# Kernel tuning notes

Hardware: AMD Instinct MI355X
Metric: run time of the kernel (lower is better)

The kernel has to match this reference:

```python
import jax, jax.numpy as jnp
import numpy as np

N_NODES = 100000
N_EDGES = 1600000
IN_DIM = 256
OUT_DIM = 128
SELF_LOOP_W = 2.0  # improved=True


def setup_inputs() -> dict:
    key = jax.random.key(0)
    ks = jax.random.split(key, 9)
    x = jax.random.normal(ks[0], (N_NODES, IN_DIM), dtype=jnp.float32)
    edge_index = jax.random.randint(ks[1], (2, N_EDGES), 0, N_NODES, dtype=jnp.int64)
    edge_weight = jax.random.uniform(ks[2], (N_EDGES,), dtype=jnp.float32)
    s1 = 1.0 / np.sqrt(IN_DIM)
    s2 = 1.0 / np.sqrt(OUT_DIM)
    W1 = jax.random.normal(ks[3], (IN_DIM, OUT_DIM), dtype=jnp.float32) * s1
    b1 = jnp.zeros((OUT_DIM,), dtype=jnp.float32)
    W_mu = jax.random.normal(ks[4], (OUT_DIM, OUT_DIM), dtype=jnp.float32) * s2
    b_mu = jnp.zeros((OUT_DIM,), dtype=jnp.float32)
    W_var = jax.random.normal(ks[5], (OUT_DIM, OUT_DIM), dtype=jnp.float32) * s2
    b_var = jnp.zeros((OUT_DIM,), dtype=jnp.float32)
    return {"x": x, "edge_index": edge_index, "edge_weight": edge_weight,
            "W1": W1, "b1": b1, "W_mu": W_mu, "b_mu": b_mu,
            "W_var": W_var, "b_var": b_var}


def _gcn_norm(edge_index, edge_weight, num_nodes):
    # add self loops with fill value 2.0 (improved=True), then symmetric norm
    loop = jnp.arange(num_nodes, dtype=edge_index.dtype)
    row = jnp.concatenate([edge_index[0], loop])
    col = jnp.concatenate([edge_index[1], loop])
    ew = jnp.concatenate([edge_weight,
                          jnp.full((num_nodes,), SELF_LOOP_W, dtype=edge_weight.dtype)])
    deg = jax.ops.segment_sum(ew, col, num_segments=num_nodes)
    dis = jnp.where(deg > 0, jax.lax.rsqrt(jnp.where(deg > 0, deg, 1.0)), 0.0)
    norm = dis[row] * ew * dis[col]
    return row, col, norm


def _gcn_conv(x, row, col, norm, W, b, num_nodes):
    xw = x @ W                      # [N, out]
    msg = xw[row] * norm[:, None]   # [E+N, out] per-edge messages
    out = jax.ops.segment_sum(msg, col, num_segments=num_nodes)
    return out + b


def reference(x, edge_index, edge_weight, W1, b1, W_mu, b_mu, W_var, b_var):
    n = x.shape[0]
    row, col, norm = _gcn_norm(edge_index, edge_weight, n)
    feat = jax.nn.relu(_gcn_conv(x, row, col, norm, W1, b1, n))
    mu = _gcn_conv(feat, row, col, norm, W_mu, b_mu, n)
    var = _gcn_conv(feat, row, col, norm, W_var, b_var, n)
    return (mu, var)
```

## Files before the change

### kernel.cpp

```cpp
#include <hip/hip_runtime.h>
#include <hip/hip_bf16.h>

#define CDIV(a,b) (((a)+(b)-1)/(b))

typedef __attribute__((ext_vector_type(8))) short short8;
typedef __attribute__((ext_vector_type(4))) float f32x4;

static __device__ inline short f2bf(float f) {
    union { __hip_bfloat16 h; short s; } u;
    u.h = __float2bfloat16(f);
    return u.s;
}
static __device__ inline ushort f2bfu(float f) { return (ushort)f2bf(f); }
static __device__ inline float bfu_lo(uint v) { return __uint_as_float(v << 16); }
static __device__ inline float bfu_hi(uint v) { return __uint_as_float(v & 0xffff0000u); }


__global__ __launch_bounds__(512) void k_init(const float* __restrict__ W1,
                                              short* __restrict__ W1t,
                                              const float* __restrict__ Wmu,
                                              const float* __restrict__ Wvar,
                                              short* __restrict__ Wcat) {
    int i = blockIdx.x * 512 + threadIdx.x;
    if (i < 128 * 256) {
        int k = i % 256, col = i / 256;
        W1t[i] = f2bf(W1[(size_t)k * 128 + col]);
    } else if (i < 2 * 128 * 256) {
        int j = i - 128 * 256;
        int k = j & 127, col = j >> 7;
        float v = (col < 128) ? Wmu[(size_t)k * 128 + col] : Wvar[(size_t)k * 128 + (col - 128)];
        Wcat[j] = f2bf(v);
    }
}


__global__ __launch_bounds__(512) void k_fat(const float* __restrict__ A,
                                             const short* __restrict__ Bt,
                                             ushort* __restrict__ C, int n, int nGB,
                                             const int* __restrict__ coli,
                                             int* __restrict__ bhist,
                                             int E, int chunkBH, int nbk, int NBH) {
    const int K = 256, KH = 128;
    __shared__ short Blds[128 * KH];
    int t = threadIdx.x;

    if (blockIdx.x >= nGB) {
        int* h = (int*)Blds;
        int b = blockIdx.x - nGB;
        for (int i = t; i < nbk; i += 512) h[i] = 0;
        __syncthreads();
        int e0 = b * chunkBH, e1 = min(E, e0 + chunkBH);
        for (int e = e0 + t; e < e1; e += 512)
            atomicAdd(&h[coli[e] >> 8], 1);
        __syncthreads();
        for (int i = t; i < nbk; i += 512)
            bhist[i * NBH + b] = h[i];
        return;
    }

    int wave = t >> 6, lane = t & 63;
    int lg = lane >> 4, lr = lane & 15;
    long row_base = (long)blockIdx.x * 256 + wave * 32;

    long ra0 = row_base + lr;      if (ra0 > n - 1) ra0 = n - 1;
    long ra1 = row_base + 16 + lr; if (ra1 > n - 1) ra1 = n - 1;

    f32x4 acc[2][8];
    #pragma unroll
    for (int i = 0; i < 2; ++i)
        #pragma unroll
        for (int j = 0; j < 8; ++j) acc[i][j] = (f32x4){0.f, 0.f, 0.f, 0.f};

    const float* pa0 = A + ra0 * K + lg * 8;
    const float* pa1 = A + ra1 * K + lg * 8;

    #pragma unroll
    for (int p = 0; p < 2; ++p) {
        if (p) __syncthreads();
        const int CHK = KH / 8;
        for (int c = t; c < 128 * CHK; c += 512) {
            int colw = c / CHK;
            int kb  = (c % CHK) * 16;
            int dst = colw * (KH * 2) + (kb ^ ((colw & 7) << 4));
            *(float4*)((char*)Blds + dst) =
                *(const float4*)((const char*)Bt + (size_t)colw * (K * 2) + p * (KH * 2) + kb);
        }
        __syncthreads();

        for (int k0 = 0; k0 < KH; k0 += 32) {
            int kg = p * KH + k0;
            float4 x0 = *(const float4*)(pa0 + kg);
            float4 x1 = *(const float4*)(pa0 + kg + 4);
            float4 y0 = *(const float4*)(pa1 + kg);
            float4 y1 = *(const float4*)(pa1 + kg + 4);
            short8 a0, a1;
            a0[0]=f2bf(x0.x); a0[1]=f2bf(x0.y); a0[2]=f2bf(x0.z); a0[3]=f2bf(x0.w);
            a0[4]=f2bf(x1.x); a0[5]=f2bf(x1.y); a0[6]=f2bf(x1.z); a0[7]=f2bf(x1.w);
            a1[0]=f2bf(y0.x); a1[1]=f2bf(y0.y); a1[2]=f2bf(y0.z); a1[3]=f2bf(y0.w);
            a1[4]=f2bf(y1.x); a1[5]=f2bf(y1.y); a1[6]=f2bf(y1.z); a1[7]=f2bf(y1.w);

            int kb = (k0 + lg * 8) * 2;
            #pragma unroll
            for (int cb = 0; cb < 8; ++cb) {
                int colm = cb * 16 + lr;
                short8 bfr = *(short8*)((char*)Blds + colm * (KH * 2) + (kb ^ ((colm & 7) << 4)));
                acc[0][cb] = __builtin_amdgcn_mfma_f32_16x16x32_bf16(a0, bfr, acc[0][cb], 0, 0, 0);
                acc[1][cb] = __builtin_amdgcn_mfma_f32_16x16x32_bf16(a1, bfr, acc[1][cb], 0, 0, 0);
            }
        }
    }

    #pragma unroll
    for (int rf = 0; rf < 2; ++rf) {
        #pragma unroll
        for (int cb = 0; cb < 8; ++cb) {
            int colm = cb * 16 + lr;
            #pragma unroll
            for (int r = 0; r < 4; ++r) {
                long row = row_base + rf * 16 + lg * 4 + r;
                if (row < n) C[row * 128 + colm] = f2bfu(acc[rf][cb][r]);
            }
        }
    }
}


__global__ __launch_bounds__(256) void kscanA(const int* __restrict__ in,
                                              int* __restrict__ out,
                                              int* __restrict__ part, int n) {
    int t = threadIdx.x;
    int base = blockIdx.x * 1024 + t * 4;
    int v0 = (base + 0 < n) ? in[base + 0] : 0;
    int v1 = (base + 1 < n) ? in[base + 1] : 0;
    int v2 = (base + 2 < n) ? in[base + 2] : 0;
    int v3 = (base + 3 < n) ? in[base + 3] : 0;
    int tsum = v0 + v1 + v2 + v3;
    int lane = t & 63, wv = t >> 6;
    int val = tsum;
    #pragma unroll
    for (int d = 1; d < 64; d <<= 1) {
        int u = __shfl_up(val, d, 64);
        if (lane >= d) val += u;
    }
    __shared__ int ws[4];
    if (lane == 63) ws[wv] = val;
    __syncthreads();
    int woff = 0;
    #pragma unroll
    for (int i = 0; i < 4; ++i) if (i < wv) woff += ws[i];
    int excl = woff + val - tsum;
    if (base + 0 < n) out[base + 0] = excl;  excl += v0;
    if (base + 1 < n) out[base + 1] = excl;  excl += v1;
    if (base + 2 < n) out[base + 2] = excl;  excl += v2;
    if (base + 3 < n) out[base + 3] = excl;
    if (t == 255) part[blockIdx.x] = woff + val;
}

__global__ __launch_bounds__(128) void kscanB(int* part, int nb) {
    int t = threadIdx.x;
    int v = (t < nb) ? part[t] : 0;
    int lane = t & 63, wv = t >> 6;
    int val = v;
    #pragma unroll
    for (int d = 1; d < 64; d <<= 1) {
        int u = __shfl_up(val, d, 64);
        if (lane >= d) val += u;
    }
    __shared__ int ws[2];
    if (lane == 63) ws[wv] = val;
    __syncthreads();
    int woff = (wv == 1) ? ws[0] : 0;
    if (t < nb) part[t] = woff + val - v;
}

__global__ __launch_bounds__(512) void k_bucket(const int* __restrict__ rowi,
                                                const int* __restrict__ coli,
                                                const float* __restrict__ ew,
                                                const int* __restrict__ excl,
                                                const int* __restrict__ part,
                                                int2* __restrict__ bxw,
                                                int E, int chunk, int nbk) {
    __shared__ int cur[512];
    int b = blockIdx.x, t = threadIdx.x, nblk = gridDim.x;
    for (int i = t; i < nbk; i += 512) cur[i] = 0;
    __syncthreads();
    int e0 = b * chunk, e1 = min(E, e0 + chunk);
    for (int e = e0 + t; e < e1; e += 512) {
        int c = coli[e];
        int bk = c >> 8;
        int idx = bk * nblk + b;
        int pos = excl[idx] + part[idx >> 10] + atomicAdd(&cur[bk], 1);
        bxw[pos] = make_int2(((c & 255) << 17) | rowi[e], __float_as_int(ew[e]));
    }
}

__global__ __launch_bounds__(512) void k_fine2(const int2* __restrict__ bxw,
                                               const int* __restrict__ excl,
                                               const int* __restrict__ part,
                                               int* __restrict__ row_ptr,
                                               float* __restrict__ dis,
                                               int E, int nblk, int n) {
    __shared__ int cnt[256], ews[256];
    __shared__ int ws2[4];
    int bk = blockIdx.x, t = threadIdx.x;
    if (t < 256) { cnt[t] = 0; ews[t] = 0; }
    __syncthreads();
    int i0 = bk * nblk;
    int s0 = excl[i0] + part[i0 >> 10];
    int s1 = E;
    if (bk + 1 < gridDim.x) {
        int i1 = (bk + 1) * nblk;
        s1 = excl[i1] + part[i1 >> 10];
    }
    for (int p = s0 + t; p < s1; p += 512) {
        int2 u = bxw[p];
        int cl = u.x >> 17;
        atomicAdd(&cnt[cl], 1);
        int q = (int)(__int_as_float(u.y) * 16777216.0f + 0.5f);
        atomicAdd(&ews[cl], q);
    }
    __syncthreads();
    int v = 0, val = 0;
    int lane = t & 63, wv = t >> 6;
    if (t < 256) {
        v = cnt[t];
        val = v;
        #pragma unroll
        for (int d = 1; d < 64; d <<= 1) {
            int u = __shfl_up(val, d, 64);
            if (lane >= d) val += u;
        }
        if (lane == 63) ws2[wv] = val;
    }
    __syncthreads();
    if (t < 256) {
        int woff = 0;
        #pragma unroll
        for (int i = 0; i < 4; ++i) if (i < wv) woff += ws2[i];
        int lexcl = woff + val - v;
        int c = bk * 256 + t;
        if (c < n) {
            row_ptr[c] = s0 + lexcl;
            dis[c] = rsqrtf(2.0f + (float)ews[t] * (1.0f / 16777216.0f));
        }
    }
    if (bk == 0 && t == 0) row_ptr[n] = E;
}

__global__ __launch_bounds__(512) void k_place(const int2* __restrict__ bxw,
                                               const int* __restrict__ excl,
                                               const int* __restrict__ part,
                                               const int* __restrict__ row_ptr,
                                               const float* __restrict__ dis,
                                               int2* __restrict__ csr,
                                               int E, int nblk, int n) {
    __shared__ int cur[256];
    int bk = blockIdx.x, t = threadIdx.x;
    if (t < 256) cur[t] = 0;
    __syncthreads();
    int i0 = bk * nblk;
    int s0 = excl[i0] + part[i0 >> 10];
    int s1 = E;
    if (bk + 1 < gridDim.x) {
        int i1 = (bk + 1) * nblk;
        s1 = excl[i1] + part[i1 >> 10];
    }
    int cbase = bk * 256;
    for (int p = s0 + t; p < s1; p += 512) {
        int2 u = bxw[p];
        int cl = u.x >> 17, r = u.x & 0x1FFFF;
        int pos = row_ptr[cbase + cl] + atomicAdd(&cur[cl], 1);
        csr[pos] = make_int2(r, __float_as_int(dis[r] * __int_as_float(u.y)));
    }
}


template<int OUTMODE>
__global__ __launch_bounds__(128) void k_agg(const uint2* __restrict__ src,
                                             const int* __restrict__ row_ptr,
                                             const int2* __restrict__ csr,
                                             const float* __restrict__ dis,
                                             const float* __restrict__ bias,
                                             uint2* __restrict__ dst, int n) {
    int wid = (blockIdx.x * 128 + threadIdx.x) >> 6;
    int lane = threadIdx.x & 63;
    int hb = lane >> 5, lc = lane & 31;
    if (wid >= n) return;
    int e0 = row_ptr[wid], e1 = row_ptr[wid + 1];

    float p00=0.f,p01=0.f,p02=0.f,p03=0.f;
    float p10=0.f,p11=0.f,p12=0.f,p13=0.f;
    float p20=0.f,p21=0.f,p22=0.f,p23=0.f;
    float p30=0.f,p31=0.f,p32=0.f,p33=0.f;

    int e = e0;
    for (; e + 7 < e1; e += 8) {
        int2 c0 = csr[e     + hb];
        int2 c1 = csr[e + 2 + hb];
        int2 c2 = csr[e + 4 + hb];
        int2 c3 = csr[e + 6 + hb];
        uint2 v0 = src[(size_t)c0.x * 32 + lc];
        uint2 v1 = src[(size_t)c1.x * 32 + lc];
        uint2 v2 = src[(size_t)c2.x * 32 + lc];
        uint2 v3 = src[(size_t)c3.x * 32 + lc];
        float w0 = __int_as_float(c0.y), w1 = __int_as_float(c1.y);
        float w2 = __int_as_float(c2.y), w3 = __int_as_float(c3.y);
        p00 += w0 * bfu_lo(v0.x); p01 += w0 * bfu_hi(v0.x);
        p02 += w0 * bfu_lo(v0.y); p03 += w0 * bfu_hi(v0.y);
        p10 += w1 * bfu_lo(v1.x); p11 += w1 * bfu_hi(v1.x);
        p12 += w1 * bfu_lo(v1.y); p13 += w1 * bfu_hi(v1.y);
        p20 += w2 * bfu_lo(v2.x); p21 += w2 * bfu_hi(v2.x);
        p22 += w2 * bfu_lo(v2.y); p23 += w2 * bfu_hi(v2.y);
        p30 += w3 * bfu_lo(v3.x); p31 += w3 * bfu_hi(v3.x);
        p32 += w3 * bfu_lo(v3.y); p33 += w3 * bfu_hi(v3.y);
    }
    for (; e + 1 < e1; e += 2) {
        int2 c = csr[e + hb];
        uint2 v = src[(size_t)c.x * 32 + lc];
        float w = __int_as_float(c.y);
        p00 += w * bfu_lo(v.x); p01 += w * bfu_hi(v.x);
        p02 += w * bfu_lo(v.y); p03 += w * bfu_hi(v.y);
    }
    if (e < e1 && hb == 0) {
        int2 c = csr[e];
        uint2 v = src[(size_t)c.x * 32 + lc];
        float w = __int_as_float(c.y);
        p10 += w * bfu_lo(v.x); p11 += w * bfu_hi(v.x);
        p12 += w * bfu_lo(v.y); p13 += w * bfu_hi(v.y);
    }

    float x0 = (p00 + p10) + (p20 + p30);
    float x1 = (p01 + p11) + (p21 + p31);
    float x2 = (p02 + p12) + (p22 + p32);
    float x3 = (p03 + p13) + (p23 + p33);
    x0 = x0 + __shfl_xor(x0, 32);
    x1 = x1 + __shfl_xor(x1, 32);
    x2 = x2 + __shfl_xor(x2, 32);
    x3 = x3 + __shfl_xor(x3, 32);

    float dc = dis[wid];
    uint2 sv = src[(size_t)wid * 32 + lc];
    float sw = 2.f * dc * dc;
    float o0 = dc * x0 + sw * bfu_lo(sv.x);
    float o1 = dc * x1 + sw * bfu_hi(sv.x);
    float o2 = dc * x2 + sw * bfu_lo(sv.y);
    float o3 = dc * x3 + sw * bfu_hi(sv.y);
    if constexpr (OUTMODE == 0) {
        float4 bv = *(const float4*)(bias + lc * 4);
        o0 += bv.x; o1 += bv.y; o2 += bv.z; o3 += bv.w;
        o0 = fmaxf(o0, 0.f); o1 = fmaxf(o1, 0.f);
        o2 = fmaxf(o2, 0.f); o3 = fmaxf(o3, 0.f);
    }
    if (hb == 0)
        dst[(size_t)wid * 32 + lc] =
            make_uint2((uint)f2bfu(o0) | ((uint)f2bfu(o1) << 16),
                       (uint)f2bfu(o2) | ((uint)f2bfu(o3) << 16));
}


__global__ __launch_bounds__(512) void k_gemm2(const short* __restrict__ A,
                                               const short* __restrict__ Bt,
                                               const float* __restrict__ bmu,
                                               const float* __restrict__ bvar,
                                               float* __restrict__ out,
                                               int n) {
    const int K = 128;
    __shared__ short Blds[256 * K];
    int t = threadIdx.x;

    const int CHK = K / 8;
    for (int c = t; c < 256 * CHK; c += 512) {
        int col = c / CHK;
        int kb  = (c % CHK) * 16;
        int dst = col * (K * 2) + (kb ^ ((col & 7) << 4));
        *(float4*)((char*)Blds + dst) =
            *(const float4*)((const char*)Bt + (size_t)col * (K * 2) + kb);
    }
    __syncthreads();

    int wave = t >> 6, lane = t & 63;
    int lg = lane >> 4, lr = lane & 15;
    int colbase = (wave & 1) * 128;
    long row_base = (long)blockIdx.x * 128 + (wave >> 1) * 32;

    long ra0 = row_base + lr;      if (ra0 > n - 1) ra0 = n - 1;
    long ra1 = row_base + 16 + lr; if (ra1 > n - 1) ra1 = n - 1;

    f32x4 acc[2][8];
    #pragma unroll
    for (int i = 0; i < 2; ++i)
        #pragma unroll
        for (int j = 0; j < 8; ++j) acc[i][j] = (f32x4){0.f, 0.f, 0.f, 0.f};

    const short* pa0 = A + ra0 * K + lg * 8;
    const short* pa1 = A + ra1 * K + lg * 8;

    #pragma unroll
    for (int k0 = 0; k0 < K; k0 += 32) {
        short8 a0 = *(const short8*)(pa0 + k0);
        short8 a1 = *(const short8*)(pa1 + k0);
        int kb = (k0 + lg * 8) * 2;
        #pragma unroll
        for (int cb = 0; cb < 8; ++cb) {
            int col = colbase + cb * 16 + lr;
            short8 b = *(short8*)((char*)Blds + col * (K * 2) + (kb ^ ((col & 7) << 4)));
            acc[0][cb] = __builtin_amdgcn_mfma_f32_16x16x32_bf16(a0, b, acc[0][cb], 0, 0, 0);
            acc[1][cb] = __builtin_amdgcn_mfma_f32_16x16x32_bf16(a1, b, acc[1][cb], 0, 0, 0);
        }
    }

    #pragma unroll
    for (int rf = 0; rf < 2; ++rf) {
        #pragma unroll
        for (int cb = 0; cb < 8; ++cb) {
            int colc = colbase + cb * 16 + lr;
            bool is_var = colc >= 128;
            int col = is_var ? colc - 128 : colc;
            float bv = is_var ? bvar[col] : bmu[col];
            size_t obase = is_var ? (size_t)n * 128 : 0;
            #pragma unroll
            for (int r = 0; r < 4; ++r) {
                long row = row_base + rf * 16 + lg * 4 + r;
                if (row < n)
                    __builtin_nontemporal_store(acc[rf][cb][r] + bv,
                                                &out[obase + (size_t)row * 128 + col]);
            }
        }
    }
}


extern "C" void kernel_launch(void* const* d_in, const int* in_sizes, int n_in,
                              void* d_out, int out_size, void* d_ws, size_t ws_size,
                              hipStream_t stream) {
    const float* x    = (const float*)d_in[0];
    const int*   ei   = (const int*)d_in[1];
    const float* ew   = (const float*)d_in[2];
    const float* W1   = (const float*)d_in[3];
    const float* b1   = (const float*)d_in[4];
    const float* Wmu  = (const float*)d_in[5];
    const float* bmu  = (const float*)d_in[6];
    const float* Wvar = (const float*)d_in[7];
    const float* bvar = (const float*)d_in[8];

    const int E = in_sizes[2];
    const int N = in_sizes[0] / 256;
    const int* rowi = ei;
    const int* coli = ei + E;

    char* base = (char*)d_ws;
    size_t off = 0;
    auto alloc = [&](size_t bytes) -> void* {
        void* p = base + off;
        off = (off + bytes + 511) & ~(size_t)511;
        return p;
    };
    const int NBH  = 256;
    const int nbk  = CDIV(N, 256);
    const int nh   = nbk * NBH;
    const int nGB  = CDIV(N, 256);
    const int chunkBH = CDIV(E, NBH);

    int*   bhist   = (int*)  alloc((size_t)nh * 4);
    int*   excl    = (int*)  alloc((size_t)nh * 4);
    int*   part    = (int*)  alloc(256 * 4);
    int2*  bxw     = (int2*) alloc((size_t)E * 8);
    int*   row_ptr = (int*)  alloc((size_t)(N + 1) * 4);
    float* dis     = (float*)alloc((size_t)N * 4);
    int2*  csr     = (int2*) alloc((size_t)E * 8);
    uint*  xw      = (uint*) alloc((size_t)N * 64 * 4);
    uint*  feat    = (uint*) alloc((size_t)N * 64 * 4);
    short* W1t     = (short*)alloc((size_t)256 * 128 * 2);
    short* Wcat    = (short*)alloc((size_t)256 * 128 * 2);
    uint*  g       = xw;

    k_init<<<CDIV(2 * 128 * 256, 512), 512, 0, stream>>>(W1, W1t, Wmu, Wvar, Wcat);

    k_fat<<<nGB + NBH, 512, 0, stream>>>(x, W1t, (ushort*)xw, N, nGB,
                                         coli, bhist, E, chunkBH, nbk, NBH);

    kscanA<<<CDIV(nh, 1024), 256, 0, stream>>>(bhist, excl, part, nh);
    kscanB<<<1, 128, 0, stream>>>(part, CDIV(nh, 1024));
    k_bucket<<<NBH, 512, 0, stream>>>(rowi, coli, ew, excl, part, bxw, E, chunkBH, nbk);
    k_fine2<<<nbk, 512, 0, stream>>>(bxw, excl, part, row_ptr, dis, E, NBH, N);
    k_place<<<nbk, 512, 0, stream>>>(bxw, excl, part, row_ptr, dis, csr, E, NBH, N);

    k_agg<0><<<CDIV(N * 64, 128), 128, 0, stream>>>((const uint2*)xw, row_ptr, csr, dis, b1, (uint2*)feat, N);
    k_agg<1><<<CDIV(N * 64, 128), 128, 0, stream>>>((const uint2*)feat, row_ptr, csr, dis, nullptr, (uint2*)g, N);
    k_gemm2<<<CDIV(N, 128), 512, 0, stream>>>((const short*)g, Wcat, bmu, bvar, (float*)d_out, N);
}
```

Measured before the change: 254.5 us.

## Drop separate part-scan kernel and halve GEMM rows per block

Removes the kscanB launch by having each consumer kernel (k_bucket, k_fine2, k_place) redundantly scan the block partial sums in shared memory. This saves one kernel launch and its serialization gap at the cost of a small duplicate scan in every block. The first GEMM in k_fat now gives each wave 16 rows instead of 32, so the grid has twice as many GEMM blocks. That raises parallelism but also doubles the LDS staging of the weight matrix relative to the useful work.

```diff
diff --git a/kernel.cpp b/kernel.cpp
--- a/kernel.cpp
+++ b/kernel.cpp
@@ -60,19 +60,15 @@
 
     int wave = t >> 6, lane = t & 63;
     int lg = lane >> 4, lr = lane & 15;
-    long row_base = (long)blockIdx.x * 256 + wave * 32;
-
-    long ra0 = row_base + lr;      if (ra0 > n - 1) ra0 = n - 1;
-    long ra1 = row_base + 16 + lr; if (ra1 > n - 1) ra1 = n - 1;
-
-    f32x4 acc[2][8];
-    #pragma unroll
-    for (int i = 0; i < 2; ++i)
-        #pragma unroll
-        for (int j = 0; j < 8; ++j) acc[i][j] = (f32x4){0.f, 0.f, 0.f, 0.f};
+    long row_base = (long)blockIdx.x * 128 + wave * 16;
+
+    long ra0 = row_base + lr; if (ra0 > n - 1) ra0 = n - 1;
+
+    f32x4 acc[8];
+    #pragma unroll
+    for (int j = 0; j < 8; ++j) acc[j] = (f32x4){0.f, 0.f, 0.f, 0.f};
 
     const float* pa0 = A + ra0 * K + lg * 8;
-    const float* pa1 = A + ra1 * K + lg * 8;
 
     #pragma unroll
     for (int p = 0; p < 2; ++p) {
@@ -91,35 +87,27 @@
             int kg = p * KH + k0;
             float4 x0 = *(const float4*)(pa0 + kg);
             float4 x1 = *(const float4*)(pa0 + kg + 4);
-            float4 y0 = *(const float4*)(pa1 + kg);
-            float4 y1 = *(const float4*)(pa1 + kg + 4);
-            short8 a0, a1;
+            short8 a0;
             a0[0]=f2bf(x0.x); a0[1]=f2bf(x0.y); a0[2]=f2bf(x0.z); a0[3]=f2bf(x0.w);
             a0[4]=f2bf(x1.x); a0[5]=f2bf(x1.y); a0[6]=f2bf(x1.z); a0[7]=f2bf(x1.w);
-            a1[0]=f2bf(y0.x); a1[1]=f2bf(y0.y); a1[2]=f2bf(y0.z); a1[3]=f2bf(y0.w);
-            a1[4]=f2bf(y1.x); a1[5]=f2bf(y1.y); a1[6]=f2bf(y1.z); a1[7]=f2bf(y1.w);
 
             int kb = (k0 + lg * 8) * 2;
             #pragma unroll
             for (int cb = 0; cb < 8; ++cb) {
                 int colm = cb * 16 + lr;
                 short8 bfr = *(short8*)((char*)Blds + colm * (KH * 2) + (kb ^ ((colm & 7) << 4)));
-                acc[0][cb] = __builtin_amdgcn_mfma_f32_16x16x32_bf16(a0, bfr, acc[0][cb], 0, 0, 0);
-                acc[1][cb] = __builtin_amdgcn_mfma_f32_16x16x32_bf16(a1, bfr, acc[1][cb], 0, 0, 0);
+                acc[cb] = __builtin_amdgcn_mfma_f32_16x16x32_bf16(a0, bfr, acc[cb], 0, 0, 0);
             }
         }
     }
 
     #pragma unroll
-    for (int rf = 0; rf < 2; ++rf) {
-        #pragma unroll
-        for (int cb = 0; cb < 8; ++cb) {
-            int colm = cb * 16 + lr;
-            #pragma unroll
-            for (int r = 0; r < 4; ++r) {
-                long row = row_base + rf * 16 + lg * 4 + r;
-                if (row < n) C[row * 128 + colm] = f2bfu(acc[rf][cb][r]);
-            }
+    for (int cb = 0; cb < 8; ++cb) {
+        int colm = cb * 16 + lr;
+        #pragma unroll
+        for (int r = 0; r < 4; ++r) {
+            long row = row_base + lg * 4 + r;
+            if (row < n) C[row * 128 + colm] = f2bfu(acc[cb][r]);
         }
     }
 }
@@ -156,61 +144,66 @@
     if (t == 255) part[blockIdx.x] = woff + val;
 }
 
-__global__ __launch_bounds__(128) void kscanB(int* part, int nb) {
+static __device__ inline void scan_parts(const int* __restrict__ part, int nparts,
+                                         int* pscan , int* wtot ) {
     int t = threadIdx.x;
-    int v = (t < nb) ? part[t] : 0;
-    int lane = t & 63, wv = t >> 6;
-    int val = v;
-    #pragma unroll
-    for (int d = 1; d < 64; d <<= 1) {
-        int u = __shfl_up(val, d, 64);
-        if (lane >= d) val += u;
-    }
-    __shared__ int ws[2];
-    if (lane == 63) ws[wv] = val;
-    __syncthreads();
-    int woff = (wv == 1) ? ws[0] : 0;
-    if (t < nb) part[t] = woff + val - v;
+    int lane = t & 63;
+    if (t < 128) {
+        int v = (t < nparts) ? part[t] : 0;
+        int val = v;
+        #pragma unroll
+        for (int d = 1; d < 64; d <<= 1) {
+            int u = __shfl_up(val, d, 64);
+            if (lane >= d) val += u;
+        }
+        if (lane == 63) wtot[t >> 6] = val;
+        pscan[t] = val - v;
+    }
+    __syncthreads();
+    if (t >= 64 && t < 128) pscan[t] += wtot[0];
+    __syncthreads();
 }
 
 __global__ __launch_bounds__(512) void k_bucket(const int* __restrict__ rowi,
                                                 const int* __restrict__ coli,
                                                 const float* __restrict__ ew,
                                                 const int* __restrict__ excl,
-                                                const int* __restrict__ part,
+                                                const int* __restrict__ part, int nparts,
                                                 int2* __restrict__ bxw,
                                                 int E, int chunk, int nbk) {
     __shared__ int cur[512];
+    __shared__ int pscan[128], wtot[2];
     int b = blockIdx.x, t = threadIdx.x, nblk = gridDim.x;
     for (int i = t; i < nbk; i += 512) cur[i] = 0;
-    __syncthreads();
+    scan_parts(part, nparts, pscan, wtot);
     int e0 = b * chunk, e1 = min(E, e0 + chunk);
     for (int e = e0 + t; e < e1; e += 512) {
         int c = coli[e];
         int bk = c >> 8;
         int idx = bk * nblk + b;
-        int pos = excl[idx] + part[idx >> 10] + atomicAdd(&cur[bk], 1);
+        int pos = excl[idx] + pscan[idx >> 10] + atomicAdd(&cur[bk], 1);
         bxw[pos] = make_int2(((c & 255) << 17) | rowi[e], __float_as_int(ew[e]));
     }
 }
 
 __global__ __launch_bounds__(512) void k_fine2(const int2* __restrict__ bxw,
                                                const int* __restrict__ excl,
-                                               const int* __restrict__ part,
+                                               const int* __restrict__ part, int nparts,
                                                int* __restrict__ row_ptr,
                                                float* __restrict__ dis,
                                                int E, int nblk, int n) {
     __shared__ int cnt[256], ews[256];
     __shared__ int ws2[4];
+    __shared__ int pscan[128], wtot[2];
     int bk = blockIdx.x, t = threadIdx.x;
     if (t < 256) { cnt[t] = 0; ews[t] = 0; }
-    __syncthreads();
+    scan_parts(part, nparts, pscan, wtot);
     int i0 = bk * nblk;
-    int s0 = excl[i0] + part[i0 >> 10];
+    int s0 = excl[i0] + pscan[i0 >> 10];
     int s1 = E;
     if (bk + 1 < gridDim.x) {
         int i1 = (bk + 1) * nblk;
-        s1 = excl[i1] + part[i1 >> 10];
+        s1 = excl[i1] + pscan[i1 >> 10];
     }
     for (int p = s0 + t; p < s1; p += 512) {
         int2 u = bxw[p];
@@ -249,21 +242,22 @@
 
 __global__ __launch_bounds__(512) void k_place(const int2* __restrict__ bxw,
                                                const int* __restrict__ excl,
-                                               const int* __restrict__ part,
+                                               const int* __restrict__ part, int nparts,
                                                const int* __restrict__ row_ptr,
                                                const float* __restrict__ dis,
                                                int2* __restrict__ csr,
                                                int E, int nblk, int n) {
     __shared__ int cur[256];
+    __shared__ int pscan[128], wtot[2];
     int bk = blockIdx.x, t = threadIdx.x;
     if (t < 256) cur[t] = 0;
-    __syncthreads();
+    scan_parts(part, nparts, pscan, wtot);
     int i0 = bk * nblk;
-    int s0 = excl[i0] + part[i0 >> 10];
+    int s0 = excl[i0] + pscan[i0 >> 10];
     int s1 = E;
     if (bk + 1 < gridDim.x) {
         int i1 = (bk + 1) * nblk;
-        s1 = excl[i1] + part[i1 >> 10];
+        s1 = excl[i1] + pscan[i1 >> 10];
     }
     int cbase = bk * 256;
     for (int p = s0 + t; p < s1; p += 512) {
@@ -458,8 +452,9 @@
     const int NBH  = 256;
     const int nbk  = CDIV(N, 256);
     const int nh   = nbk * NBH;
-    const int nGB  = CDIV(N, 256);
+    const int nGB  = CDIV(N, 128);
     const int chunkBH = CDIV(E, NBH);
+    const int nparts  = CDIV(nh, 1024);
 
     int*   bhist   = (int*)  alloc((size_t)nh * 4);
     int*   excl    = (int*)  alloc((size_t)nh * 4);
@@ -480,10 +475,9 @@
                                          coli, bhist, E, chunkBH, nbk, NBH);
 
     kscanA<<<CDIV(nh, 1024), 256, 0, stream>>>(bhist, excl, part, nh);
-    kscanB<<<1, 128, 0, stream>>>(part, CDIV(nh, 1024));
-    k_bucket<<<NBH, 512, 0, stream>>>(rowi, coli, ew, excl, part, bxw, E, chunkBH, nbk);
-    k_fine2<<<nbk, 512, 0, stream>>>(bxw, excl, part, row_ptr, dis, E, NBH, N);
-    k_place<<<nbk, 512, 0, stream>>>(bxw, excl, part, row_ptr, dis, csr, E, NBH, N);
+    k_bucket<<<NBH, 512, 0, stream>>>(rowi, coli, ew, excl, part, nparts, bxw, E, chunkBH, nbk);
+    k_fine2<<<nbk, 512, 0, stream>>>(bxw, excl, part, nparts, row_ptr, dis, E, NBH, N);
+    k_place<<<nbk, 512, 0, stream>>>(bxw, excl, part, nparts, row_ptr, dis, csr, E, NBH, N);
 
     k_agg<0><<<CDIV(N * 64, 128), 128, 0, stream>>>((const uint2*)xw, row_ptr, csr, dis, b1, (uint2*)feat, N);
     k_agg<1><<<CDIV(N * 64, 128), 128, 0, stream>>>((const uint2*)feat, row_ptr, csr, dis, nullptr, (uint2*)g, N);
```

Measured after the change: 257.6 us. About the same (+1.2%).
